# Kernel tuning notes

Measured on AMD Instinct MI355X. Metric: run time of the kernel, lower is better.

## Reference

```python
import jax, jax.numpy as jnp
import numpy as np
from jax import lax

N, T, H, W, E = 512, 10, 40, 40, 8192

def _conv2d(x, w, b):
    y = lax.conv_general_dilated(x, w, (1, 1), 'SAME',
                                 dimension_numbers=('NCHW', 'OIHW', 'NCHW'))
    return y + b[None, :, None, None]

def _bn_per_t(x, g, b, eps=1e-5):
    # x: (N, T, C, H, W); torch training-mode BN stats computed per timestep (loop over t in original)
    mu = x.mean(axis=(0, 3, 4), keepdims=True)
    var = x.var(axis=(0, 3, 4), keepdims=True)
    return g[None, None, :, None, None] * (x - mu) * lax.rsqrt(var + eps) + b[None, None, :, None, None]

def _maxpool2(x):
    return lax.reduce_window(x, -jnp.inf, lax.max, (1, 1, 2, 2), (1, 1, 2, 2), 'VALID')

def _cnn(x, w1, b1, g1, be1, w2, b2, g2, be2):
    # conv3x3 -> BN -> relu -> maxpool2 -> conv3x3 -> BN -> relu -> adaptive avgpool(5,5); x: (N,T,Cin,H,W)
    n, t, c, h, w = x.shape
    y = _conv2d(x.reshape(n * t, c, h, w), w1, b1).reshape(n, t, 16, h, w)
    y = jax.nn.relu(_bn_per_t(y, g1, be1))
    y = _maxpool2(y.reshape(n * t, 16, h, w))
    y = _conv2d(y, w2, b2)
    co = w2.shape[0]
    y = jax.nn.relu(_bn_per_t(y.reshape(n, t, co, h // 2, w // 2), g2, be2))
    k = (h // 2) // 5  # 20 -> 5 is a uniform 4x4 average pool
    y = y.reshape(n, t, co, 5, k, 5, k).mean(axis=(4, 6))
    return y.reshape(n, t, co * 25)

def _sage(x, src, dst, wl, bl, wr):
    # PyG SAGEConv(aggr='max'): lin_l(max-aggregated neighbor feats) + lin_r(x); x: (T,N,F)
    t, n, f = x.shape
    msgs = x[:, src]                                               # (T,E,F) gather
    agg = jnp.full((t, n, f), -jnp.inf, x.dtype).at[:, dst].max(msgs)
    agg = jnp.where(jnp.isfinite(agg), agg, 0.0)                   # isolated nodes -> 0 (PyG convention)
    return jnp.einsum('tnf,of->tno', agg, wl) + bl + jnp.einsum('tnf,of->tno', x, wr)

def _lstm_last(x, wih, whh, bih, bhh):
    # x: (T,N,F); torch gate order i,f,g,o; returns final hidden state h_T
    t, n, _ = x.shape
    hdim = whh.shape[1]
    def step(carry, xt):
        h, c = carry
        z = xt @ wih.T + bih + h @ whh.T + bhh
        i, f, g, o = jnp.split(z, 4, axis=-1)
        c = jax.nn.sigmoid(f) * c + jax.nn.sigmoid(i) * jnp.tanh(g)
        h = jax.nn.sigmoid(o) * jnp.tanh(c)
        return (h, c), None
    init = (jnp.zeros((n, hdim), x.dtype), jnp.zeros((n, hdim), x.dtype))
    (h, _), _ = lax.scan(step, init, x)
    return h

def _forward(veg, cwsi, irrigation, edge_index, vw1, vb1, vg1, vbe1, vw2, vb2, vg2, vbe2,
             cw1, cb1, cg1, cbe1, cw2, cb2, cg2, cbe2, emb,
             s1_wl, s1_bl, s1_wr, s2_wl, s2_bl, s2_wr, wih, whh, bih, bhh, fcw, fcb):
    vfeat = _cnn(veg, vw1, vb1, vg1, vbe1, vw2, vb2, vg2, vbe2)    # (N,T,400)
    cfeat = _cnn(cwsi, cw1, cb1, cg1, cbe1, cw2, cb2, cg2, cbe2)   # (N,T,200)
    ifeat = emb[irrigation]                                        # (N,T,16)
    feats = jnp.concatenate([vfeat, cfeat, ifeat], axis=-1).transpose(1, 0, 2)  # (T,N,616)
    src, dst = edge_index[0], edge_index[1]
    x = jax.nn.relu(_sage(feats, src, dst, s1_wl, s1_bl, s1_wr))
    x = jax.nn.relu(_sage(x, src, dst, s2_wl, s2_bl, s2_wr))       # (T,N,32)
    h = _lstm_last(x, wih, whh, bih, bhh)                          # (N,64)
    return h @ fcw.T + fcb                                         # (N,1)

def setup_inputs():
    key = jax.random.key(0)
    ks = jax.random.split(key, 16)
    w = lambda i, shape: jax.random.normal(ks[i], shape, jnp.float32) * 0.05
    return dict(
        veg=jax.random.normal(ks[0], (N, T, 5, H, W), jnp.float32),
        cwsi=jax.random.normal(ks[1], (N, T, 1, H, W), jnp.float32),
        irrigation=jax.random.randint(ks[2], (N, T), 0, 3, jnp.int32),
        edge_index=jax.random.randint(ks[3], (2, E), 0, N, jnp.int32),
        vw1=w(4, (16, 5, 3, 3)), vb1=jnp.zeros(16), vg1=jnp.ones(16), vbe1=jnp.zeros(16),
        vw2=w(5, (16, 16, 3, 3)), vb2=jnp.zeros(16), vg2=jnp.ones(16), vbe2=jnp.zeros(16),
        cw1=w(6, (16, 1, 3, 3)), cb1=jnp.zeros(16), cg1=jnp.ones(16), cbe1=jnp.zeros(16),
        cw2=w(7, (8, 16, 3, 3)), cb2=jnp.zeros(8), cg2=jnp.ones(8), cbe2=jnp.zeros(8),
        emb=jax.random.normal(ks[8], (3, 16), jnp.float32),
        s1_wl=w(9, (64, 616)), s1_bl=jnp.zeros(64), s1_wr=w(10, (64, 616)),
        s2_wl=w(11, (32, 64)), s2_bl=jnp.zeros(32), s2_wr=w(12, (32, 64)),
        wih=w(13, (256, 32)), whh=w(14, (256, 64)), bih=jnp.zeros(256), bhh=jnp.zeros(256),
        fcw=w(15, (1, 64)), fcb=jnp.zeros(1),
    )

def reference(veg, cwsi, irrigation, edge_index, vw1, vb1, vg1, vbe1, vw2, vb2, vg2, vbe2,
              cw1, cb1, cg1, cbe1, cw2, cb2, cg2, cbe2, emb,
              s1_wl, s1_bl, s1_wr, s2_wl, s2_bl, s2_wr, wih, whh, bih, bhh, fcw, fcb):
    return _forward(veg, cwsi, irrigation, edge_index, vw1, vb1, vg1, vbe1, vw2, vb2, vg2, vbe2,
                    cw1, cb1, cg1, cbe1, cw2, cb2, cg2, cbe2, emb,
                    s1_wl, s1_bl, s1_wr, s2_wl, s2_bl, s2_wr, wih, whh, bih, bhh, fcw, fcb)
```

## Files before the change

kernel.cpp:

```cpp
#include <hip/hip_runtime.h>
#include <math.h>

#define NBATCH 512
#define TSTEPS 10
#define NIMG   5120
#define FEAT   616
#define NEDGE  8192

__device__ __forceinline__ float sigf(float x){ return 1.f/(1.f + expf(-x)); }

__global__ void prep_kernel(const float* __restrict__ s1wl, const float* __restrict__ s1wr,
                            const float* __restrict__ s2wl, const float* __restrict__ s2wr,
                            const float* __restrict__ wih,  const float* __restrict__ whh,
                            const float* __restrict__ vw1,  const float* __restrict__ cw1,
                            const float* __restrict__ vw2,  const float* __restrict__ cw2,
                            float* __restrict__ wlT, float* __restrict__ wrT,
                            float* __restrict__ wl2T, float* __restrict__ wr2T,
                            float* __restrict__ wihT, float* __restrict__ whhT,
                            float* __restrict__ w1vT, float* __restrict__ w1cT,
                            float* __restrict__ w2vT, float* __restrict__ w2cT,
                            double* __restrict__ stats)
{
  int idx = blockIdx.x*256 + threadIdx.x;
  if (idx < 39424){ wlT[(idx%616)*64 + idx/616] = s1wl[idx]; return; }
  idx -= 39424;
  if (idx < 39424){ wrT[(idx%616)*64 + idx/616] = s1wr[idx]; return; }
  idx -= 39424;
  if (idx < 2048){ wl2T[(idx%64)*32 + idx/64] = s2wl[idx]; return; }
  idx -= 2048;
  if (idx < 2048){ wr2T[(idx%64)*32 + idx/64] = s2wr[idx]; return; }
  idx -= 2048;
  if (idx < 8192){ wihT[(idx%32)*256 + idx/32] = wih[idx]; return; }
  idx -= 8192;
  if (idx < 16384){ whhT[(idx%64)*256 + idx/64] = whh[idx]; return; }
  idx -= 16384;
  if (idx < 720){
    int co = idx & 15, k = (idx >> 4) % 9, ci = idx / 144;
    w1vT[idx] = vw1[(co*5 + ci)*9 + k]; return;
  }
  idx -= 720;
  if (idx < 144){
    int co = idx & 15, k = idx >> 4;
    w1cT[idx] = cw1[co*9 + k]; return;
  }
  idx -= 144;
  if (idx < 2304){
    int co = idx & 15, k = (idx >> 4) % 9, ci = idx / 144;
    w2vT[idx] = vw2[(co*16 + ci)*9 + k]; return;
  }
  idx -= 2304;
  if (idx < 1152){
    int co = idx & 7, k = (idx >> 3) % 9, ci = idx / 72;
    w2cT[idx] = cw2[(co*16 + ci)*9 + k]; return;
  }
  idx -= 1152;
  if (idx < 1280){ stats[idx] = 0.0; }
}

__global__ void csr_kernel(const int* __restrict__ edges, int* __restrict__ row_start,
                           int* __restrict__ adj)
{
  __shared__ int cnt_s[512];
  __shared__ int scan_s[512];
  const int tid = threadIdx.x;
  const int* src = edges;
  const int* dst = edges + NEDGE;
  cnt_s[tid] = 0;
  __syncthreads();
  for (int e = tid; e < NEDGE; e += 512) atomicAdd(&cnt_s[dst[e]], 1);
  __syncthreads();
  int v = cnt_s[tid];
  scan_s[tid] = v;
  __syncthreads();
  for (int off = 1; off < 512; off <<= 1){
    int add = (tid >= off) ? scan_s[tid - off] : 0;
    __syncthreads();
    scan_s[tid] += add;
    __syncthreads();
  }
  int start = scan_s[tid] - v;
  row_start[tid] = start;
  if (tid == 511) row_start[512] = scan_s[511];
  cnt_s[tid] = start;
  __syncthreads();
  for (int e = tid; e < NEDGE; e += 512){
    int d = dst[e];
    int pos = atomicAdd(&cnt_s[d], 1);
    adj[pos] = src[e];
  }
}

template<int CIN>
__launch_bounds__(256)
__global__ void conv1_kernel(const float* __restrict__ in, const float* __restrict__ wT,
                             double* __restrict__ stats, float* __restrict__ premax)
{
  constexpr int INT = CIN*936;
  constexpr int SMF = (INT > 4608) ? INT : 4608;
  __shared__ __attribute__((aligned(16))) float smem[SMF];
  float* in_t = smem;
  float* red  = smem;
  float* plds = smem + 2048;
  const int tid = threadIdx.x;
  const int bid = blockIdx.x;
  const int img = bid / 3, strip = bid % 3;
  const int y0 = strip * 16;
  const int t = img % TSTEPS;
  const float* imgp = in + (size_t)img * CIN * 1600;

  for (int ci = 0; ci < CIN; ci++){
    const float* ip = imgp + ci*1600;
    float* ot = &in_t[ci*936];
    for (int idx = tid; idx < 864; idx += 256){
      int r = idx / 48, w = idx % 48;
      int g = w / 12, c = w % 12;
      int gy = y0 + r - 1, gx = g*10 + c - 1;
      float v = 0.f;
      if ((unsigned)gy < 40u && (unsigned)gx < 40u) v = ip[gy*40 + gx];
      ot[r*52 + g*12 + c] = v;
    }
  }
  __syncthreads();

  const int lane = tid & 63;
  const int co0 = __builtin_amdgcn_readfirstlane(tid >> 6) * 4;
  const int row = lane & 15, g = lane >> 4;
  const int gy = y0 + row;
  const bool act = gy < 40;

  float acc[10][4];
  #pragma unroll
  for (int i = 0; i < 10; i++)
    #pragma unroll
    for (int j = 0; j < 4; j++) acc[i][j] = 0.f;

  for (int ci = 0; ci < CIN; ci++){
    const float* wp = wT + ci*144 + co0;
    float4 sw[9];
    #pragma unroll
    for (int k = 0; k < 9; k++) sw[k] = *(const float4*)(wp + k*16);
    const float* rbase = &in_t[ci*936 + row*52 + g*12];
    #pragma unroll
    for (int dy = 0; dy < 3; dy++){
      float v[12];
      const float* rp = rbase + dy*52;
      const float4 a = *(const float4*)rp;
      const float4 b = *(const float4*)(rp + 4);
      const float4 c = *(const float4*)(rp + 8);
      v[0] = a.x; v[1]  = a.y; v[2]  = a.z; v[3]  = a.w;
      v[4] = b.x; v[5]  = b.y; v[6]  = b.z; v[7]  = b.w;
      v[8] = c.x; v[9]  = c.y; v[10] = c.z; v[11] = c.w;
      #pragma unroll
      for (int dx = 0; dx < 3; dx++){
        const float4 wv = sw[dy*3 + dx];
        #pragma unroll
        for (int p = 0; p < 10; p++){
          float iv = v[p + dx];
          acc[p][0] += iv*wv.x; acc[p][1] += iv*wv.y;
          acc[p][2] += iv*wv.z; acc[p][3] += iv*wv.w;
        }
      }
    }
  }

  __syncthreads();

  #pragma unroll
  for (int cl = 0; cl < 4; cl++){
    float s = 0.f, q = 0.f;
    #pragma unroll
    for (int p = 0; p < 10; p++){
      float a = acc[p][cl];
      s += a; q += a*a;
    }
    red[(co0 + cl)*64 + lane]        = act ? s : 0.f;
    red[1024 + (co0 + cl)*64 + lane] = act ? q : 0.f;
  }
  #pragma unroll
  for (int cl = 0; cl < 4; cl++){
    float hp[5];
    #pragma unroll
    for (int j = 0; j < 5; j++) hp[j] = fmaxf(acc[2*j][cl], acc[2*j + 1][cl]);
    float op[5];
    #pragma unroll
    for (int j = 0; j < 5; j++) op[j] = __shfl_xor(hp[j], 1, 64);
    if (!(row & 1)){
      #pragma unroll
      for (int j = 0; j < 5; j++)
        plds[(co0 + cl)*160 + (row >> 1)*20 + g*5 + j] = fmaxf(hp[j], op[j]);
    }
  }
  __syncthreads();

  {
    const int co = tid >> 4, seg = tid & 15;
    float vs = 0.f, vq = 0.f;
    #pragma unroll
    for (int j = 0; j < 4; j++){
      vs += red[co*64 + seg*4 + j];
      vq += red[1024 + co*64 + seg*4 + j];
    }
    #pragma unroll
    for (int off = 8; off > 0; off >>= 1){
      vs += __shfl_down(vs, off, 16);
      vq += __shfl_down(vq, off, 16);
    }
    if (seg == 0){
      atomicAdd(&stats[(t*16 + co)*2 + 0], (double)vs);
      atomicAdd(&stats[(t*16 + co)*2 + 1], (double)vq);
    }
  }
  {
    float* pb = premax + (size_t)img*6400;
    #pragma unroll
    for (int k = 0; k < 10; k++){
      int idx = tid + k*256;
      int co = idx / 160, rem = idx % 160;
      int py = rem / 20, col = rem % 20;
      int gpy = strip*8 + py;
      if (gpy < 20) pb[co*400 + gpy*20 + col] = plds[idx];
    }
  }
}

template<int CO>
__launch_bounds__(256)
__global__ void conv2_kernel(float* __restrict__ pooled, const float* __restrict__ wT,
                             const float* __restrict__ bnp1, double* __restrict__ stats)
{
  constexpr int R = (CO == 16) ? 2 : 1;
  constexpr int P = (20/R) * 5;
  __shared__ __attribute__((aligned(16))) float in_t[16*528];
  const int tid = threadIdx.x;
  const int img = blockIdx.x;
  const int t = img % TSTEPS;
  const size_t ib = (size_t)img * 6400;

  {
    const int r0 = tid / 24, c0 = tid % 24;
    for (int ci = 0; ci < 16; ci++){
      const float sc = bnp1[(t*16 + ci)*2 + 0];
      const float sh = bnp1[(t*16 + ci)*2 + 1];
      const float* ip = pooled + ib + ci*400;
      float* ot = &in_t[ci*528];
      int r = r0, c = c0;
      #pragma unroll
      for (int k = 0; k < 3; k++){
        int idx = tid + k*256;
        if (idx < 528){
          int gy = r - 1, gx = c - 1;
          float v = 0.f;
          if ((unsigned)gy < 20u && (unsigned)gx < 20u)
            v = fmaxf(sc*ip[gy*20 + gx] + sh, 0.f);
          ot[r*24 + c] = v;
        }
        r += 10; c += 16; if (c >= 24){ c -= 24; r += 1; }
      }
    }
  }
  __syncthreads();

  const int cog = (CO == 16) ? __builtin_amdgcn_readfirstlane(tid >> 6)
                             : __builtin_amdgcn_readfirstlane(tid >> 7);
  const int q   = (CO == 16) ? (tid & 63) : (tid & 127);
  const bool act = q < P;
  const int x4 = (q % 5) * 4, yb = (q / 5) * R;
  const int co0 = cog * 4;
  float acc[R][4][4];
  #pragma unroll
  for (int rr = 0; rr < R; rr++)
    #pragma unroll
    for (int i = 0; i < 4; i++)
      #pragma unroll
      for (int j = 0; j < 4; j++) acc[rr][i][j] = 0.f;

  if (act){
    for (int ci = 0; ci < 16; ci++){
      const float* wp = wT + ci*9*CO + co0;
      float4 sw[9];
      #pragma unroll
      for (int k = 0; k < 9; k++) sw[k] = *(const float4*)(wp + k*CO);
      float v[R + 2][6];
      #pragma unroll
      for (int r = 0; r < R + 2; r++){
        const float* rp = &in_t[ci*528 + (yb + r)*24 + x4];
        const float4 a = *(const float4*)rp;
        const float2 b = *(const float2*)(rp + 4);
        v[r][0] = a.x; v[r][1] = a.y; v[r][2] = a.z; v[r][3] = a.w;
        v[r][4] = b.x; v[r][5] = b.y;
      }
      #pragma unroll
      for (int dy = 0; dy < 3; dy++)
        #pragma unroll
        for (int dx = 0; dx < 3; dx++){
          const float4 wv = sw[dy*3 + dx];
          #pragma unroll
          for (int rr = 0; rr < R; rr++){
            #pragma unroll
            for (int px = 0; px < 4; px++){
              float iv = v[rr + dy][px + dx];
              acc[rr][px][0] += iv*wv.x; acc[rr][px][1] += iv*wv.y;
              acc[rr][px][2] += iv*wv.z; acc[rr][px][3] += iv*wv.w;
            }
          }
        }
    }
    #pragma unroll
    for (int cl = 0; cl < 4; cl++)
      #pragma unroll
      for (int rr = 0; rr < R; rr++){
        float4 o4;
        o4.x = acc[rr][0][cl]; o4.y = acc[rr][1][cl];
        o4.z = acc[rr][2][cl]; o4.w = acc[rr][3][cl];
        *(float4*)&pooled[ib + (co0 + cl)*400 + (yb + rr)*20 + x4] = o4;
      }
  }
  __syncthreads();

  if (act){
    #pragma unroll
    for (int cl = 0; cl < 4; cl++){
      float s = 0.f, qq = 0.f;
      #pragma unroll
      for (int rr = 0; rr < R; rr++)
        #pragma unroll
        for (int px = 0; px < 4; px++){
          float a = acc[rr][px][cl];
          s += a; qq += a*a;
        }
      in_t[(co0 + cl)*P + q]            = s;
      in_t[CO*P + (co0 + cl)*P + q]     = qq;
    }
  }
  __syncthreads();
  if (tid < CO*8){
    int co = tid >> 3, seg = tid & 7;
    float vs = 0.f, vq = 0.f;
    for (int j = seg; j < P; j += 8){
      vs += in_t[co*P + j];
      vq += in_t[CO*P + co*P + j];
    }
    #pragma unroll
    for (int off = 4; off > 0; off >>= 1){
      vs += __shfl_down(vs, off, 8);
      vq += __shfl_down(vq, off, 8);
    }
    if (seg == 0){
      atomicAdd(&stats[(t*CO + co)*2 + 0], (double)vs);
      atomicAdd(&stats[(t*CO + co)*2 + 1], (double)vq);
    }
  }
}

template<int CO>
__global__ void bnavg_kernel(const float* __restrict__ raw, const float* __restrict__ bnp,
                             float* __restrict__ feats, int featBase)
{
  const int img = blockIdx.x;
  const int t = img % TSTEPS, n = img / TSTEPS;
  for (int idx = threadIdx.x; idx < CO*25; idx += 256){
    int co = idx / 25, q = idx % 25, py = q / 5, px = q % 5;
    float sc = bnp[(t*CO + co)*2 + 0];
    float sh = bnp[(t*CO + co)*2 + 1];
    const float* base = raw + (size_t)img*6400 + co*400 + (py*4)*20 + px*4;
    float s = 0.f;
    #pragma unroll
    for (int r = 0; r < 4; r++){
      float4 v = *(const float4*)(base + r*20);
      s += fmaxf(v.x*sc + sh, 0.f) + fmaxf(v.y*sc + sh, 0.f)
         + fmaxf(v.z*sc + sh, 0.f) + fmaxf(v.w*sc + sh, 0.f);
    }
    feats[(size_t)(t*NBATCH + n)*FEAT + featBase + idx] = s * 0.0625f;
  }
}

__global__ void bn_param_kernel(const double* __restrict__ stats, float* __restrict__ bnp,
                                const float* __restrict__ g, const float* __restrict__ be,
                                int C, double invCnt)
{
  int idx = threadIdx.x;
  if (idx < TSTEPS*C){
    int c = idx % C;
    double mean = stats[idx*2] * invCnt;
    double var  = stats[idx*2 + 1] * invCnt - mean*mean;
    if (var < 0.0) var = 0.0;
    double sc = (double)g[c] / sqrt(var + 1e-5);
    bnp[idx*2]     = (float)sc;
    bnp[idx*2 + 1] = be[c] - (float)(mean * sc);
  }
}

__global__ void emb_kernel(const int* __restrict__ irr, const float* __restrict__ emb,
                           float* __restrict__ feats)
{
  int idx = blockIdx.x*256 + threadIdx.x;
  if (idx >= NBATCH*TSTEPS*16) return;
  int k = idx & 15;
  int nt = idx >> 4;
  int t = nt % TSTEPS, n = nt / TSTEPS;
  feats[(size_t)(t*NBATCH + n)*FEAT + 600 + k] = emb[irr[nt]*16 + k];
}

__global__ void agg_kernel(const float* __restrict__ feats, const int* __restrict__ row_start,
                           const int* __restrict__ adj, float* __restrict__ agg)
{
  __shared__ int adjs[192];
  const int bid = blockIdx.x;
  const int t = bid / NBATCH, n = bid % NBATCH;
  const int tid = threadIdx.x;
  const int rs = row_start[n], re = row_start[n + 1];
  const int deg = re - rs;
  for (int i = tid; i < deg && i < 192; i += 256) adjs[i] = adj[rs + i];
  __syncthreads();
  const float* fb = feats + (size_t)t*NBATCH*FEAT;
  float* ab = agg + (size_t)(t*NBATCH + n)*FEAT;
  for (int f = tid; f < FEAT; f += 256){
    float m = -1e30f;
    for (int j = 0; j < deg; j++){
      int s = (j < 192) ? adjs[j] : adj[rs + j];
      m = fmaxf(m, fb[(size_t)s*FEAT + f]);
    }
    ab[f] = (deg > 0) ? m : 0.f;
  }
}

__launch_bounds__(256)
__global__ void sage1_kernel(const float* __restrict__ feats, const float* __restrict__ agg,
                             const float* __restrict__ wlT, const float* __restrict__ wrT,
                             const float* __restrict__ bl, float* __restrict__ x1)
{
  __shared__ float xr[4][616];
  __shared__ float ar[4][616];
  const int tid = threadIdx.x;
  const int bid = blockIdx.x;
  for (int idx = tid; idx < 4*616; idx += 256){
    int r = idx / 616, f = idx % 616;
    size_t row = (size_t)bid*4 + r;
    xr[r][f] = feats[row*FEAT + f];
    ar[r][f] = agg[row*FEAT + f];
  }
  __syncthreads();
  const int wid = tid >> 6, o = tid & 63;
  const int row = bid*4 + wid;
  float acc = bl[o];
  #pragma unroll 4
  for (int f = 0; f < 616; f++){
    acc += ar[wid][f]*wlT[f*64 + o] + xr[wid][f]*wrT[f*64 + o];
  }
  x1[(size_t)row*64 + o] = fmaxf(acc, 0.f);
}

__launch_bounds__(64)
__global__ void sage2_kernel(const float* __restrict__ x1, const int* __restrict__ row_start,
                             const int* __restrict__ adj, const float* __restrict__ wl2T,
                             const float* __restrict__ wr2T, const float* __restrict__ bl2,
                             float* __restrict__ x2)
{
  __shared__ float am[64], xm[64];
  __shared__ int adjs[192];
  const int bid = blockIdx.x;
  const int t = bid / NBATCH, n = bid % NBATCH;
  const int lane = threadIdx.x;
  const int rs = row_start[n], re = row_start[n + 1];
  const int deg = re - rs;
  for (int i = lane; i < deg && i < 192; i += 64) adjs[i] = adj[rs + i];
  __syncthreads();
  const float* xb = x1 + (size_t)t*NBATCH*64;
  float m = -1e30f;
  for (int j = 0; j < deg; j++){
    int s = (j < 192) ? adjs[j] : adj[rs + j];
    m = fmaxf(m, xb[s*64 + lane]);
  }
  am[lane] = (deg > 0) ? m : 0.f;
  xm[lane] = xb[n*64 + lane];
  __syncthreads();
  if (lane < 32){
    float acc = bl2[lane];
    #pragma unroll 4
    for (int f = 0; f < 64; f++){
      acc += am[f]*wl2T[f*32 + lane] + xm[f]*wr2T[f*32 + lane];
    }
    x2[(size_t)(t*NBATCH + n)*32 + lane] = fmaxf(acc, 0.f);
  }
}

__launch_bounds__(256)
__global__ void lstm_kernel(const float* __restrict__ x2, const float* __restrict__ wihT,
                            const float* __restrict__ whhT, const float* __restrict__ bih,
                            const float* __restrict__ bhh, const float* __restrict__ fcw,
                            const float* __restrict__ fcb, float* __restrict__ out)
{
  __shared__ float xb[32], hb[64], cbuf[64], zb[256];
  const int n = blockIdx.x;
  const int tid = threadIdx.x;
  if (tid < 64){ hb[tid] = 0.f; cbuf[tid] = 0.f; }
  __syncthreads();
  const float bsum = bih[tid] + bhh[tid];
  for (int t = 0; t < TSTEPS; t++){
    if (tid < 32) xb[tid] = x2[(size_t)(t*NBATCH + n)*32 + tid];
    __syncthreads();
    float acc = bsum;
    #pragma unroll 8
    for (int k = 0; k < 32; k++) acc += xb[k]*wihT[k*256 + tid];
    #pragma unroll 8
    for (int k = 0; k < 64; k++) acc += hb[k]*whhT[k*256 + tid];
    zb[tid] = acc;
    __syncthreads();
    if (tid < 64){
      float zi = zb[tid], zf = zb[64 + tid], zg = zb[128 + tid], zo = zb[192 + tid];
      float c = sigf(zf)*cbuf[tid] + sigf(zi)*tanhf(zg);
      cbuf[tid] = c;
      hb[tid] = sigf(zo)*tanhf(c);
    }
    __syncthreads();
  }
  if (tid < 64){
    float v = hb[tid]*fcw[tid];
    #pragma unroll
    for (int off = 32; off > 0; off >>= 1) v += __shfl_down(v, off, 64);
    if (tid == 0) out[n] = v + fcb[0];
  }
}

extern "C" void kernel_launch(void* const* d_in, const int* in_sizes, int n_in,
                              void* d_out, int out_size, void* d_ws, size_t ws_size,
                              hipStream_t stream)
{
  const float* veg  = (const float*)d_in[0];
  const float* cwsi = (const float*)d_in[1];
  const int*   irr  = (const int*)d_in[2];
  const int*   eidx = (const int*)d_in[3];
  const float* vw1  = (const float*)d_in[4];
  const float* vg1  = (const float*)d_in[6];
  const float* vbe1 = (const float*)d_in[7];
  const float* vw2  = (const float*)d_in[8];
  const float* vg2  = (const float*)d_in[10];
  const float* vbe2 = (const float*)d_in[11];
  const float* cw1  = (const float*)d_in[12];
  const float* cg1  = (const float*)d_in[14];
  const float* cbe1 = (const float*)d_in[15];
  const float* cw2  = (const float*)d_in[16];
  const float* cg2  = (const float*)d_in[18];
  const float* cbe2 = (const float*)d_in[19];
  const float* emb  = (const float*)d_in[20];
  const float* s1wl = (const float*)d_in[21];
  const float* s1bl = (const float*)d_in[22];
  const float* s1wr = (const float*)d_in[23];
  const float* s2wl = (const float*)d_in[24];
  const float* s2bl = (const float*)d_in[25];
  const float* s2wr = (const float*)d_in[26];
  const float* wih  = (const float*)d_in[27];
  const float* whh  = (const float*)d_in[28];
  const float* bih  = (const float*)d_in[29];
  const float* bhh  = (const float*)d_in[30];
  const float* fcw  = (const float*)d_in[31];
  const float* fcb  = (const float*)d_in[32];
  float* out = (float*)d_out;

  float* ws = (float*)d_ws;
  size_t off = 0;
  float* pooled = ws + off; off += (size_t)NIMG*6400;
  float* feats  = ws + off; off += (size_t)NIMG*FEAT;
  float* agg1   = ws + off; off += (size_t)NIMG*FEAT;
  float* x1     = ws + off; off += (size_t)NIMG*64;
  float* x2     = ws + off; off += (size_t)NIMG*32;
  float* wlT    = ws + off; off += 39424;
  float* wrT    = ws + off; off += 39424;
  float* wl2T   = ws + off; off += 2048;
  float* wr2T   = ws + off; off += 2048;
  float* wihT   = ws + off; off += 8192;
  float* whhT   = ws + off; off += 16384;
  float* w1vT   = ws + off; off += 720;
  float* w1cT   = ws + off; off += 144;
  float* w2vT   = ws + off; off += 2304;
  float* w2cT   = ws + off; off += 1152;
  off = (off + 1) & ~(size_t)1;
  double* stats = (double*)(ws + off); off += 2560;
  float* bnp    = ws + off; off += 1280;
  int* row_start= (int*)(ws + off); off += 513;
  int* adj      = (int*)(ws + off); off += 8192;
  (void)in_sizes; (void)n_in; (void)out_size; (void)ws_size;

  prep_kernel<<<442, 256, 0, stream>>>(s1wl, s1wr, s2wl, s2wr, wih, whh,
                                       vw1, cw1, vw2, cw2,
                                       wlT, wrT, wl2T, wr2T, wihT, whhT,
                                       w1vT, w1cT, w2vT, w2cT, stats);
  csr_kernel<<<1, 512, 0, stream>>>(eidx, row_start, adj);

  double* stV1 = stats;        float* bnV1 = bnp;
  double* stV2 = stats + 320;  float* bnV2 = bnp + 320;
  double* stC1 = stats + 640;  float* bnC1 = bnp + 640;
  double* stC2 = stats + 960;  float* bnC2 = bnp + 960;

  conv1_kernel<5><<<NIMG*3, 256, 0, stream>>>(veg, w1vT, stV1, pooled);
  bn_param_kernel<<<1, 256, 0, stream>>>(stV1, bnV1, vg1, vbe1, 16, 1.0/(512.0*1600.0));
  conv2_kernel<16><<<NIMG, 256, 0, stream>>>(pooled, w2vT, bnV1, stV2);
  bn_param_kernel<<<1, 256, 0, stream>>>(stV2, bnV2, vg2, vbe2, 16, 1.0/(512.0*400.0));
  bnavg_kernel<16><<<NIMG, 256, 0, stream>>>(pooled, bnV2, feats, 0);

  conv1_kernel<1><<<NIMG*3, 256, 0, stream>>>(cwsi, w1cT, stC1, pooled);
  bn_param_kernel<<<1, 256, 0, stream>>>(stC1, bnC1, cg1, cbe1, 16, 1.0/(512.0*1600.0));
  conv2_kernel<8><<<NIMG, 256, 0, stream>>>(pooled, w2cT, bnC1, stC2);
  bn_param_kernel<<<1, 256, 0, stream>>>(stC2, bnC2, cg2, cbe2, 8, 1.0/(512.0*400.0));
  bnavg_kernel<8><<<NIMG, 256, 0, stream>>>(pooled, bnC2, feats, 400);

  emb_kernel<<<(NBATCH*TSTEPS*16 + 255)/256, 256, 0, stream>>>(irr, emb, feats);
  agg_kernel<<<NIMG, 256, 0, stream>>>(feats, row_start, adj, agg1);
  sage1_kernel<<<NIMG/4, 256, 0, stream>>>(feats, agg1, wlT, wrT, s1bl, x1);
  sage2_kernel<<<NIMG, 64, 0, stream>>>(x1, row_start, adj, wl2T, wr2T, s2bl, x2);
  lstm_kernel<<<NBATCH, 256, 0, stream>>>(x2, wihT, whhT, bih, bhh, fcw, fcb, out);
}
```

Baseline: 760.4 us.

## Fuse BN parameter computation, embedding, and neighbor max-aggregation into consumer kernels

Removes the four single-block bn_param launches by having conv2 and bnavg compute the BatchNorm scale and shift per block from the accumulated stats. It folds the embedding write into the cwsi bnavg kernel and moves the SAGE max-aggregation into sage1, so the separate agg1 buffer no longer has to be written and read back. This cuts launch count and global traffic. In exchange, the BN parameters are recomputed redundantly in every block, and sage1 now does the irregular neighbor gather with only 1280 blocks, so that gather runs with less parallelism than before.

```diff
diff --git a/kernel.cpp b/kernel.cpp
--- a/kernel.cpp
+++ b/kernel.cpp
@@ -6,6 +6,9 @@
 #define NIMG   5120
 #define FEAT   616
 #define NEDGE  8192
+
+#define INV1 (1.0/(512.0*1600.0))
+#define INV2 (1.0/(512.0*400.0))
 
 __device__ __forceinline__ float sigf(float x){ return 1.f/(1.f + expf(-x)); }
 
@@ -226,21 +229,34 @@
 template<int CO>
 __launch_bounds__(256)
 __global__ void conv2_kernel(float* __restrict__ pooled, const float* __restrict__ wT,
-                             const float* __restrict__ bnp1, double* __restrict__ stats)
+                             const double* __restrict__ stats1,
+                             const float* __restrict__ g1, const float* __restrict__ be1,
+                             double* __restrict__ stats)
 {
   constexpr int R = (CO == 16) ? 2 : 1;
   constexpr int P = (20/R) * 5;
   __shared__ __attribute__((aligned(16))) float in_t[16*528];
+  __shared__ float bnp_s[32];
   const int tid = threadIdx.x;
   const int img = blockIdx.x;
   const int t = img % TSTEPS;
   const size_t ib = (size_t)img * 6400;
 
+  if (tid < 16){
+    double mean = stats1[(t*16 + tid)*2 + 0] * INV1;
+    double var  = stats1[(t*16 + tid)*2 + 1] * INV1 - mean*mean;
+    if (var < 0.0) var = 0.0;
+    double sc = (double)g1[tid] / sqrt(var + 1e-5);
+    bnp_s[tid*2 + 0] = (float)sc;
+    bnp_s[tid*2 + 1] = be1[tid] - (float)(mean * sc);
+  }
+  __syncthreads();
+
   {
     const int r0 = tid / 24, c0 = tid % 24;
     for (int ci = 0; ci < 16; ci++){
-      const float sc = bnp1[(t*16 + ci)*2 + 0];
-      const float sh = bnp1[(t*16 + ci)*2 + 1];
+      const float sc = bnp_s[ci*2 + 0];
+      const float sh = bnp_s[ci*2 + 1];
       const float* ip = pooled + ib + ci*400;
       float* ot = &in_t[ci*528];
       int r = r0, c = c0;
@@ -352,16 +368,30 @@
   }
 }
 
-template<int CO>
-__global__ void bnavg_kernel(const float* __restrict__ raw, const float* __restrict__ bnp,
+template<int CO, int EMB>
+__global__ void bnavg_kernel(const float* __restrict__ raw,
+                             const double* __restrict__ stats2,
+                             const float* __restrict__ g2, const float* __restrict__ be2,
+                             const int* __restrict__ irr, const float* __restrict__ emb,
                              float* __restrict__ feats, int featBase)
 {
+  __shared__ float bnp_s[32];
   const int img = blockIdx.x;
   const int t = img % TSTEPS, n = img / TSTEPS;
-  for (int idx = threadIdx.x; idx < CO*25; idx += 256){
+  const int tid = threadIdx.x;
+  if (tid < CO){
+    double mean = stats2[(t*CO + tid)*2 + 0] * INV2;
+    double var  = stats2[(t*CO + tid)*2 + 1] * INV2 - mean*mean;
+    if (var < 0.0) var = 0.0;
+    double sc = (double)g2[tid] / sqrt(var + 1e-5);
+    bnp_s[tid*2 + 0] = (float)sc;
+    bnp_s[tid*2 + 1] = be2[tid] - (float)(mean * sc);
+  }
+  __syncthreads();
+  for (int idx = tid; idx < CO*25; idx += 256){
     int co = idx / 25, q = idx % 25, py = q / 5, px = q % 5;
-    float sc = bnp[(t*CO + co)*2 + 0];
-    float sh = bnp[(t*CO + co)*2 + 1];
+    float sc = bnp_s[co*2 + 0];
+    float sh = bnp_s[co*2 + 1];
     const float* base = raw + (size_t)img*6400 + co*400 + (py*4)*20 + px*4;
     float s = 0.f;
     #pragma unroll
@@ -372,60 +402,14 @@
     }
     feats[(size_t)(t*NBATCH + n)*FEAT + featBase + idx] = s * 0.0625f;
   }
-}
-
-__global__ void bn_param_kernel(const double* __restrict__ stats, float* __restrict__ bnp,
-                                const float* __restrict__ g, const float* __restrict__ be,
-                                int C, double invCnt)
-{
-  int idx = threadIdx.x;
-  if (idx < TSTEPS*C){
-    int c = idx % C;
-    double mean = stats[idx*2] * invCnt;
-    double var  = stats[idx*2 + 1] * invCnt - mean*mean;
-    if (var < 0.0) var = 0.0;
-    double sc = (double)g[c] / sqrt(var + 1e-5);
-    bnp[idx*2]     = (float)sc;
-    bnp[idx*2 + 1] = be[c] - (float)(mean * sc);
-  }
-}
-
-__global__ void emb_kernel(const int* __restrict__ irr, const float* __restrict__ emb,
-                           float* __restrict__ feats)
-{
-  int idx = blockIdx.x*256 + threadIdx.x;
-  if (idx >= NBATCH*TSTEPS*16) return;
-  int k = idx & 15;
-  int nt = idx >> 4;
-  int t = nt % TSTEPS, n = nt / TSTEPS;
-  feats[(size_t)(t*NBATCH + n)*FEAT + 600 + k] = emb[irr[nt]*16 + k];
-}
-
-__global__ void agg_kernel(const float* __restrict__ feats, const int* __restrict__ row_start,
-                           const int* __restrict__ adj, float* __restrict__ agg)
-{
-  __shared__ int adjs[192];
-  const int bid = blockIdx.x;
-  const int t = bid / NBATCH, n = bid % NBATCH;
-  const int tid = threadIdx.x;
-  const int rs = row_start[n], re = row_start[n + 1];
-  const int deg = re - rs;
-  for (int i = tid; i < deg && i < 192; i += 256) adjs[i] = adj[rs + i];
-  __syncthreads();
-  const float* fb = feats + (size_t)t*NBATCH*FEAT;
-  float* ab = agg + (size_t)(t*NBATCH + n)*FEAT;
-  for (int f = tid; f < FEAT; f += 256){
-    float m = -1e30f;
-    for (int j = 0; j < deg; j++){
-      int s = (j < 192) ? adjs[j] : adj[rs + j];
-      m = fmaxf(m, fb[(size_t)s*FEAT + f]);
-    }
-    ab[f] = (deg > 0) ? m : 0.f;
+  if (EMB && tid < 16){
+    feats[(size_t)(t*NBATCH + n)*FEAT + 600 + tid] = emb[irr[img]*16 + tid];
   }
 }
 
 __launch_bounds__(256)
-__global__ void sage1_kernel(const float* __restrict__ feats, const float* __restrict__ agg,
+__global__ void sage1_kernel(const float* __restrict__ feats,
+                             const int* __restrict__ row_start, const int* __restrict__ adj,
                              const float* __restrict__ wlT, const float* __restrict__ wrT,
                              const float* __restrict__ bl, float* __restrict__ x1)
 {
@@ -433,15 +417,31 @@
   __shared__ float ar[4][616];
   const int tid = threadIdx.x;
   const int bid = blockIdx.x;
+  const int row0 = bid*4;
+  const int t = row0 / NBATCH;
+  const int n0 = row0 - t*NBATCH;
+  const float* fb = feats + (size_t)t*NBATCH*FEAT;
+
   for (int idx = tid; idx < 4*616; idx += 256){
     int r = idx / 616, f = idx % 616;
-    size_t row = (size_t)bid*4 + r;
-    xr[r][f] = feats[row*FEAT + f];
-    ar[r][f] = agg[row*FEAT + f];
+    xr[r][f] = feats[(size_t)(row0 + r)*FEAT + f];
+  }
+  for (int r = 0; r < 4; r++){
+    const int n = n0 + r;
+    const int rs = row_start[n], re = row_start[n + 1];
+    const int deg = re - rs;
+    for (int f = tid; f < 616; f += 256){
+      float m = -1e30f;
+      for (int j = 0; j < deg; j++){
+        int s = adj[rs + j];
+        m = fmaxf(m, fb[(size_t)s*FEAT + f]);
+      }
+      ar[r][f] = (deg > 0) ? m : 0.f;
+    }
   }
   __syncthreads();
   const int wid = tid >> 6, o = tid & 63;
-  const int row = bid*4 + wid;
+  const int row = row0 + wid;
   float acc = bl[o];
   #pragma unroll 4
   for (int f = 0; f < 616; f++){
@@ -561,7 +561,6 @@
   size_t off = 0;
   float* pooled = ws + off; off += (size_t)NIMG*6400;
   float* feats  = ws + off; off += (size_t)NIMG*FEAT;
-  float* agg1   = ws + off; off += (size_t)NIMG*FEAT;
   float* x1     = ws + off; off += (size_t)NIMG*64;
   float* x2     = ws + off; off += (size_t)NIMG*32;
   float* wlT    = ws + off; off += 39424;
@@ -576,7 +575,6 @@
   float* w2cT   = ws + off; off += 1152;
   off = (off + 1) & ~(size_t)1;
   double* stats = (double*)(ws + off); off += 2560;
-  float* bnp    = ws + off; off += 1280;
   int* row_start= (int*)(ws + off); off += 513;
   int* adj      = (int*)(ws + off); off += 8192;
   (void)in_sizes; (void)n_in; (void)out_size; (void)ws_size;
@@ -587,26 +585,22 @@
                                        w1vT, w1cT, w2vT, w2cT, stats);
   csr_kernel<<<1, 512, 0, stream>>>(eidx, row_start, adj);
 
-  double* stV1 = stats;        float* bnV1 = bnp;
-  double* stV2 = stats + 320;  float* bnV2 = bnp + 320;
-  double* stC1 = stats + 640;  float* bnC1 = bnp + 640;
-  double* stC2 = stats + 960;  float* bnC2 = bnp + 960;
+  double* stV1 = stats;
+  double* stV2 = stats + 320;
+  double* stC1 = stats + 640;
+  double* stC2 = stats + 960;
 
   conv1_kernel<5><<<NIMG*3, 256, 0, stream>>>(veg, w1vT, stV1, pooled);
-  bn_param_kernel<<<1, 256, 0, stream>>>(stV1, bnV1, vg1, vbe1, 16, 1.0/(512.0*1600.0));
-  conv2_kernel<16><<<NIMG, 256, 0, stream>>>(pooled, w2vT, bnV1, stV2);
-  bn_param_kernel<<<1, 256, 0, stream>>>(stV2, bnV2, vg2, vbe2, 16, 1.0/(512.0*400.0));
-  bnavg_kernel<16><<<NIMG, 256, 0, stream>>>(pooled, bnV2, feats, 0);
+  conv2_kernel<16><<<NIMG, 256, 0, stream>>>(pooled, w2vT, stV1, vg1, vbe1, stV2);
+  bnavg_kernel<16,0><<<NIMG, 256, 0, stream>>>(pooled, stV2, vg2, vbe2,
+                                               irr, emb, feats, 0);
 
   conv1_kernel<1><<<NIMG*3, 256, 0, stream>>>(cwsi, w1cT, stC1, pooled);
-  bn_param_kernel<<<1, 256, 0, stream>>>(stC1, bnC1, cg1, cbe1, 16, 1.0/(512.0*1600.0));
-  conv2_kernel<8><<<NIMG, 256, 0, stream>>>(pooled, w2cT, bnC1, stC2);
-  bn_param_kernel<<<1, 256, 0, stream>>>(stC2, bnC2, cg2, cbe2, 8, 1.0/(512.0*400.0));
-  bnavg_kernel<8><<<NIMG, 256, 0, stream>>>(pooled, bnC2, feats, 400);
-
-  emb_kernel<<<(NBATCH*TSTEPS*16 + 255)/256, 256, 0, stream>>>(irr, emb, feats);
-  agg_kernel<<<NIMG, 256, 0, stream>>>(feats, row_start, adj, agg1);
-  sage1_kernel<<<NIMG/4, 256, 0, stream>>>(feats, agg1, wlT, wrT, s1bl, x1);
+  conv2_kernel<8><<<NIMG, 256, 0, stream>>>(pooled, w2cT, stC1, cg1, cbe1, stC2);
+  bnavg_kernel<8,1><<<NIMG, 256, 0, stream>>>(pooled, stC2, cg2, cbe2,
+                                              irr, emb, feats, 400);
+
+  sage1_kernel<<<NIMG/4, 256, 0, stream>>>(feats, row_start, adj, wlT, wrT, s1bl, x1);
   sage2_kernel<<<NIMG, 64, 0, stream>>>(x1, row_start, adj, wl2T, wr2T, s2bl, x2);
   lstm_kernel<<<NBATCH, 256, 0, stream>>>(x2, wihT, whhT, bih, bhh, fcw, fcb, out);
 }
```

After: 751.8 us (median of 2 runs). No clear change (-1.1%).
